# Performance work log

Hardware: AMD Instinct MI355X
Metric: run time of the kernel (lower is better)

Reference implementation:

```python
import jax, jax.numpy as jnp
import numpy as np

N_IN = 512
SCALE = 0  # s / n_in**scale == s when scale=0

def setup_inputs() -> dict:
    key = jax.random.key(0)
    k1, k2, k3, k4 = jax.random.split(key, 4)
    B, S, D = 4, 128, N_IN
    x = jax.random.normal(k1, (B, S, D), dtype=jnp.float32)
    y = jax.random.normal(k2, (B, S, D), dtype=jnp.float32)
    z = jax.random.normal(k3, (B, S, D), dtype=jnp.float32)
    # weight: (n_out, n_in + bias_x, n_in, n_in + bias_y)
    weight = jax.random.normal(k4, (1, D + 1, D, D + 1), dtype=jnp.float32) * 0.02
    return {"x": x, "y": y, "z": z, "weight": weight}

def reference(x, y, z, weight):
    # append bias-1 column to x and y (bias_x=bias_y=True)
    ones = jnp.ones_like(x[..., :1])
    xb = jnp.concatenate([x, ones], axis=-1)           # [b, s, n_in+1]
    yb = jnp.concatenate([y, jnp.ones_like(y[..., :1])], axis=-1)
    # w = z^T W : [b, o, z, i, j]
    w = jnp.einsum('bzk,oikj->bozij', z, weight)
    # s(x,y,z) = x^T (z^T W) y : [b, o, z, x, y]
    s = jnp.einsum('bxi,bozij,byj->bozxy', xb, w, yb)
    # n_out == 1 -> squeeze channel dim; scale == 0 -> divide by n_in**0 == 1
    return jnp.squeeze(s, axis=1) / (N_IN ** SCALE)
```

## Files before the change

### kernel.cpp

```cpp
#include <hip/hip_runtime.h>
#include <stdint.h>


typedef __attribute__((ext_vector_type(8))) short bf16x8;
typedef __attribute__((ext_vector_type(4))) float f32x4;

__device__ __forceinline__ unsigned short f2bf(float f) {
    unsigned int u = __float_as_uint(f);
    u += 0x7fffu + ((u >> 16) & 1u);
    return (unsigned short)(u >> 16);
}

__device__ __forceinline__ void gload_lds16(const void* g, void* l) {
    __builtin_amdgcn_global_load_lds((const __attribute__((address_space(1))) void*)g,
                                     (__attribute__((address_space(3))) void*)l, 16, 0, 0);
}

__global__ __launch_bounds__(256) void k_cast(const float* __restrict__ x,
    const float* __restrict__ y, const float* __restrict__ z,
    unsigned short* __restrict__ xbf, unsigned short* __restrict__ ybf,
    unsigned short* __restrict__ zbf)
{
    int t = blockIdx.x * 256 + threadIdx.x;
    int arr = t >> 15;
    int off = (t & 32767) * 8;
    const float* src = (arr == 0) ? x : (arr == 1) ? y : z;
    unsigned short* dst = (arr == 0) ? xbf : (arr == 1) ? ybf : zbf;
    float4 a = *(const float4*)(src + off);
    float4 b = *(const float4*)(src + off + 4);
    uint4 o;
    o.x = f2bf(a.x) | ((unsigned)f2bf(a.y) << 16);
    o.y = f2bf(a.z) | ((unsigned)f2bf(a.w) << 16);
    o.z = f2bf(b.x) | ((unsigned)f2bf(b.y) << 16);
    o.w = f2bf(b.z) | ((unsigned)f2bf(b.w) << 16);
    *(uint4*)(dst + off) = o;
}

__global__ __launch_bounds__(256) void k_edge(const float* __restrict__ z,
    const float* __restrict__ w, float* __restrict__ a_arr,
    float* __restrict__ c_arr, float* __restrict__ d_arr)
{
    __shared__ float Zs[64][33];
    __shared__ float Bs[32][65];
    int t = threadIdx.x;
    int mb = blockIdx.x % 17, bzb = blockIdx.x / 17;
    int tr = t >> 4, tc = t & 15;
    float acc[4][4] = {};
    for (int k0 = 0; k0 < 512; k0 += 32) {
        __syncthreads();
        {   int row = t >> 2, ko = (t & 3) * 8;
            const float* p = z + (bzb * 64 + row) * 512 + k0 + ko;
            float4 v0 = ((const float4*)p)[0], v1 = ((const float4*)p)[1];
            Zs[row][ko + 0] = v0.x; Zs[row][ko + 1] = v0.y; Zs[row][ko + 2] = v0.z; Zs[row][ko + 3] = v0.w;
            Zs[row][ko + 4] = v1.x; Zs[row][ko + 5] = v1.y; Zs[row][ko + 6] = v1.z; Zs[row][ko + 7] = v1.w;
        }
        {   int kr = t >> 3, mo = (t & 7) * 8;
            for (int e = 0; e < 8; ++e) {
                int m = mb * 64 + mo + e;
                float v = 0.f;
                int krow = k0 + kr;
                if (m < 512)        v = w[(m * 512 + krow) * 513 + 512];
                else if (m < 1024)  v = w[(262144 + krow) * 513 + (m - 512)];
                else if (m == 1024) v = w[(262144 + krow) * 513 + 512];
                Bs[kr][mo + e] = v;
            }
        }
        __syncthreads();
        for (int kk = 0; kk < 32; ++kk) {
            float zr[4], br[4];
            for (int r = 0; r < 4; ++r) zr[r] = Zs[tr * 4 + r][kk];
            for (int c = 0; c < 4; ++c) br[c] = Bs[kk][tc * 4 + c];
            for (int r = 0; r < 4; ++r)
                for (int c = 0; c < 4; ++c) acc[r][c] += zr[r] * br[c];
        }
    }
    for (int r = 0; r < 4; ++r)
        for (int c = 0; c < 4; ++c) {
            int bz = bzb * 64 + tr * 4 + r;
            int m = mb * 64 + tc * 4 + c;
            if (m < 512)        a_arr[bz * 512 + m] = acc[r][c];
            else if (m < 1024)  c_arr[bz * 512 + (m - 512)] = acc[r][c];
            else if (m == 1024) d_arr[bz] = acc[r][c];
        }
}

__global__ __launch_bounds__(512, 2) void k_gemm1(const unsigned short* __restrict__ zbf,
    const float* __restrict__ w, unsigned short* __restrict__ Mws,
    int i0, int chi)
{
    extern __shared__ unsigned char smem[];
    unsigned char* Zb0 = smem;
    unsigned char* Zb1 = smem + 32768;
    unsigned char* Bb0 = smem + 65536;
    unsigned char* Bb1 = smem + 73728;

    int nwg = gridDim.x;
    int cpx = nwg >> 3;
    int bid = blockIdx.x;
    int swz = (bid & 7) * cpx + (bid >> 3);
    int iloc = swz >> 2, jb = swz & 3;
    int j0 = jb * 128;
    int t = threadIdx.x, wid = t >> 6, lane = t & 63;
    int bzg = wid >> 1, jg = wid & 1;
    int l15 = lane & 15, l4 = lane >> 4;

    int arow = lane >> 2;
    int akc  = (lane & 3) ^ ((lane >> 3) & 3);
    const unsigned short* zbase = zbf + (size_t)(wid * 64 + arow) * 512 + akc * 8;

    int jB = t & 127, kq8 = t >> 7;
    const float* wb = w + (size_t)(i0 + iloc) * 262656 + (size_t)(kq8 * 8) * 513 + j0 + jB;
    int bwoff = jB * 64 + (((kq8 >> 1) ^ ((jB >> 1) & 3)) * 16) + 0;
    bwoff = jB * 64 + ((kq8 ^ ((jB >> 1) & 3)) * 16);

    int aoff = (bzg * 128 + l15) * 64 + ((l4 ^ ((l15 >> 1) & 3)) * 16);
    int boff = (jg * 64 + l15) * 64 + ((l4 ^ ((l15 >> 1) & 3)) * 16);

    f32x4 acc[8][4];
    #pragma unroll
    for (int mt = 0; mt < 8; ++mt)
        #pragma unroll
        for (int nt = 0; nt < 4; ++nt) acc[mt][nt] = (f32x4){0.f, 0.f, 0.f, 0.f};

    float wr[2][8];

    #pragma unroll
    for (int q = 0; q < 4; ++q)
        gload_lds16(zbase + q * 8192, Zb0 + wid * 4096 + q * 1024);
    {
        #pragma unroll
        for (int e = 0; e < 8; ++e) wr[0][e] = wb[(size_t)e * 513];
        const float* wp = wb + (size_t)32 * 513;
        #pragma unroll
        for (int e = 0; e < 8; ++e) wr[1][e] = wp[(size_t)e * 513];
        uint4 pk;
        pk.x = f2bf(wr[0][0]) | ((unsigned)f2bf(wr[0][1]) << 16);
        pk.y = f2bf(wr[0][2]) | ((unsigned)f2bf(wr[0][3]) << 16);
        pk.z = f2bf(wr[0][4]) | ((unsigned)f2bf(wr[0][5]) << 16);
        pk.w = f2bf(wr[0][6]) | ((unsigned)f2bf(wr[0][7]) << 16);
        *(uint4*)(Bb0 + bwoff) = pk;
    }
    asm volatile("s_waitcnt lgkmcnt(0)" ::: "memory");
    __builtin_amdgcn_s_barrier();
    __builtin_amdgcn_sched_barrier(0);

    #pragma unroll
    for (int ks = 0; ks < 16; ++ks) {
        const int cur = ks & 1;
        unsigned char* Zcur  = cur ? Zb1 : Zb0;
        unsigned char* Znext = cur ? Zb0 : Zb1;
        unsigned char* Bcur  = cur ? Bb1 : Bb0;
        unsigned char* Bnext = cur ? Bb0 : Bb1;

        if (ks < 15) {
            #pragma unroll
            for (int q = 0; q < 4; ++q)
                gload_lds16(zbase + (ks + 1) * 32 + q * 8192, Znext + wid * 4096 + q * 1024);
        }
        if (ks < 14) {
            const float* wp = wb + (size_t)(ks + 2) * 32 * 513;
            #pragma unroll
            for (int e = 0; e < 8; ++e) wr[cur][e] = wp[(size_t)e * 513];
        }
        bf16x8 bfr[4];
        #pragma unroll
        for (int nt = 0; nt < 4; ++nt)
            bfr[nt] = *(const bf16x8*)(Bcur + boff + nt * 1024);
        #pragma unroll
        for (int mt = 0; mt < 8; ++mt) {
            bf16x8 afr = *(const bf16x8*)(Zcur + aoff + mt * 1024);
            #pragma unroll
            for (int nt = 0; nt < 4; ++nt)
                acc[mt][nt] = __builtin_amdgcn_mfma_f32_16x16x32_bf16(afr, bfr[nt], acc[mt][nt], 0, 0, 0);
        }
        if (ks < 15) {
            uint4 pk;
            pk.x = f2bf(wr[cur ^ 1][0]) | ((unsigned)f2bf(wr[cur ^ 1][1]) << 16);
            pk.y = f2bf(wr[cur ^ 1][2]) | ((unsigned)f2bf(wr[cur ^ 1][3]) << 16);
            pk.z = f2bf(wr[cur ^ 1][4]) | ((unsigned)f2bf(wr[cur ^ 1][5]) << 16);
            pk.w = f2bf(wr[cur ^ 1][6]) | ((unsigned)f2bf(wr[cur ^ 1][7]) << 16);
            *(uint4*)(Bnext + bwoff) = pk;
        }
        if (ks < 14) {
            asm volatile("s_waitcnt vmcnt(8) lgkmcnt(0)" ::: "memory");
        } else if (ks == 14) {
            asm volatile("s_waitcnt vmcnt(0) lgkmcnt(0)" ::: "memory");
        }
        if (ks < 15) {
            __builtin_amdgcn_s_barrier();
            __builtin_amdgcn_sched_barrier(0);
        }
    }

    size_t mrow = (size_t)chi * 512;
    #pragma unroll
    for (int mt = 0; mt < 8; ++mt)
        #pragma unroll
        for (int nt = 0; nt < 4; ++nt)
            #pragma unroll
            for (int r = 0; r < 4; ++r) {
                int bz = bzg * 128 + mt * 16 + l4 * 4 + r;
                int j  = j0 + jg * 64 + nt * 16 + l15;
                Mws[(size_t)bz * mrow + (size_t)iloc * 512 + j] = f2bf(acc[mt][nt][r]);
            }
}

__global__ __launch_bounds__(512) void k_fuse(const unsigned short* __restrict__ xbf,
    const unsigned short* __restrict__ ybf, const unsigned short* __restrict__ Mws,
    const float* __restrict__ xf, const float* __restrict__ yf,
    const float* __restrict__ a_arr, const float* __restrict__ c_arr,
    const float* __restrict__ d_arr, float* __restrict__ out,
    int i0, int nib, int chi, int first)
{
    __shared__ unsigned short Xlds[128 * 72];
    __shared__ unsigned short Ylds[128 * 72];
    __shared__ unsigned short Mlds[64 * 72];
    __shared__ unsigned short Rlds[128 * 72];
    int bid = blockIdx.x;
    int bz = (bid & 7) * 64 + (bid >> 3);
    int b = bz >> 7;
    int t = threadIdx.x;
    int wid = t >> 6, lane = t & 63;
    int l15 = lane & 15, l4 = lane >> 4;
    int xg = wid >> 2, yg = wid & 3;

    f32x4 acc[4][2];
    if (first) {
        float* part = (float*)Xlds;
        float* uv = (float*)Ylds;
        int xr = t & 127, q = t >> 7;
        {   const float* xp = xf + (size_t)(b * 128 + xr) * 512 + q * 128;
            const float* ap = a_arr + bz * 512 + q * 128;
            float s = 0.f;
            for (int ii = 0; ii < 128; ++ii) s += xp[ii] * ap[ii];
            part[q * 128 + xr] = s;
        }
        __syncthreads();
        if (t < 128) uv[t] = part[t] + part[128 + t] + part[256 + t] + part[384 + t];
        __syncthreads();
        {   const float* yp = yf + (size_t)(b * 128 + xr) * 512 + q * 128;
            const float* cp = c_arr + bz * 512 + q * 128;
            float s = 0.f;
            for (int ii = 0; ii < 128; ++ii) s += yp[ii] * cp[ii];
            part[q * 128 + xr] = s;
        }
        __syncthreads();
        if (t < 128) uv[128 + t] = part[t] + part[128 + t] + part[256 + t] + part[384 + t];
        __syncthreads();
        float dv = d_arr[bz];
        for (int mt = 0; mt < 4; ++mt)
            for (int nt = 0; nt < 2; ++nt) {
                int y = yg * 32 + nt * 16 + l15;
                for (int r = 0; r < 4; ++r) {
                    int x = xg * 64 + mt * 16 + l4 * 4 + r;
                    acc[mt][nt][r] = uv[x] + uv[128 + y] + dv;
                }
            }
    } else {
        for (int mt = 0; mt < 4; ++mt) for (int nt = 0; nt < 2; ++nt) acc[mt][nt] = (f32x4){0.f,0.f,0.f,0.f};
    }

    for (int ibl = 0; ibl < nib; ++ibl) {
        __syncthreads();
        {   int xr = t >> 2, io = (t & 3) * 16;
            const uint4* src = (const uint4*)(xbf + (size_t)(b * 128 + xr) * 512 + i0 + ibl * 64 + io);
            uint4 v0 = src[0], v1 = src[1];
            uint4* dst = (uint4*)(Xlds + xr * 72 + io);
            dst[0] = v0; dst[1] = v1;
        }
        f32x4 accR[2][2];
        for (int mt = 0; mt < 2; ++mt) for (int nt = 0; nt < 2; ++nt) accR[mt][nt] = (f32x4){0.f,0.f,0.f,0.f};

        for (int jbk = 0; jbk < 8; ++jbk) {
            __syncthreads();
            {   int yr = t >> 2, jo = (t & 3) * 16;
                const uint4* src = (const uint4*)(ybf + (size_t)(b * 128 + yr) * 512 + jbk * 64 + jo);
                uint4 v0 = src[0], v1 = src[1];
                uint4* dst = (uint4*)(Ylds + yr * 72 + jo);
                dst[0] = v0; dst[1] = v1;
            }
            {   int ir = t >> 3, jo = (t & 7) * 8;
                uint4 v = *(const uint4*)(Mws + (size_t)bz * ((size_t)chi * 512)
                                              + (size_t)(ibl * 64 + ir) * 512 + jbk * 64 + jo);
                *(uint4*)(Mlds + ir * 72 + jo) = v;
            }
            __syncthreads();
            for (int kf = 0; kf < 2; ++kf) {
                bf16x8 bfr[2];
                for (int nt = 0; nt < 2; ++nt) {
                    int y = yg * 32 + nt * 16 + l15;
                    bfr[nt] = *(const bf16x8*)(Ylds + y * 72 + kf * 32 + l4 * 8);
                }
                for (int mt = 0; mt < 2; ++mt) {
                    int ir = xg * 32 + mt * 16 + l15;
                    bf16x8 afr = *(const bf16x8*)(Mlds + ir * 72 + kf * 32 + l4 * 8);
                    accR[mt][0] = __builtin_amdgcn_mfma_f32_16x16x32_bf16(afr, bfr[0], accR[mt][0], 0, 0, 0);
                    accR[mt][1] = __builtin_amdgcn_mfma_f32_16x16x32_bf16(afr, bfr[1], accR[mt][1], 0, 0, 0);
                }
            }
        }
        for (int mt = 0; mt < 2; ++mt)
            for (int nt = 0; nt < 2; ++nt) {
                int y = yg * 32 + nt * 16 + l15;
                int ir = xg * 32 + mt * 16 + l4 * 4;
                unsigned p0 = f2bf(accR[mt][nt][0]) | ((unsigned)f2bf(accR[mt][nt][1]) << 16);
                unsigned p1 = f2bf(accR[mt][nt][2]) | ((unsigned)f2bf(accR[mt][nt][3]) << 16);
                *(uint2*)(Rlds + y * 72 + ir) = make_uint2(p0, p1);
            }
        __syncthreads();
        for (int kf = 0; kf < 2; ++kf) {
            bf16x8 bfr[2];
            for (int nt = 0; nt < 2; ++nt) {
                int y = yg * 32 + nt * 16 + l15;
                bfr[nt] = *(const bf16x8*)(Rlds + y * 72 + kf * 32 + l4 * 8);
            }
            for (int mt = 0; mt < 4; ++mt) {
                int x = xg * 64 + mt * 16 + l15;
                bf16x8 afr = *(const bf16x8*)(Xlds + x * 72 + kf * 32 + l4 * 8);
                acc[mt][0] = __builtin_amdgcn_mfma_f32_16x16x32_bf16(afr, bfr[0], acc[mt][0], 0, 0, 0);
                acc[mt][1] = __builtin_amdgcn_mfma_f32_16x16x32_bf16(afr, bfr[1], acc[mt][1], 0, 0, 0);
            }
        }
    }
    float* op = out + (size_t)bz * 16384;
    for (int mt = 0; mt < 4; ++mt)
        for (int nt = 0; nt < 2; ++nt)
            for (int r = 0; r < 4; ++r) {
                int x = xg * 64 + mt * 16 + l4 * 4 + r;
                int y = yg * 32 + nt * 16 + l15;
                if (first) op[x * 128 + y] = acc[mt][nt][r];
                else       op[x * 128 + y] += acc[mt][nt][r];
            }
}

extern "C" void kernel_launch(void* const* d_in, const int* in_sizes, int n_in,
                              void* d_out, int out_size, void* d_ws, size_t ws_size,
                              hipStream_t stream)
{
    const float* x = (const float*)d_in[0];
    const float* y = (const float*)d_in[1];
    const float* z = (const float*)d_in[2];
    const float* w = (const float*)d_in[3];
    float* out = (float*)d_out;
    char* ws = (char*)d_ws;

    unsigned short* xbf = (unsigned short*)(ws + 0);
    unsigned short* ybf = (unsigned short*)(ws + 524288);
    unsigned short* zbf = (unsigned short*)(ws + 1048576);
    float* a_arr = (float*)(ws + 1572864);
    float* c_arr = (float*)(ws + 2621440);
    float* d_arr = (float*)(ws + 3670016);
    unsigned short* Mws = (unsigned short*)(ws + 3674112);

    size_t avail = (ws_size > 3674112) ? ws_size - 3674112 : 0;
    int chi = 512;
    while (chi > 64 && (size_t)chi * 524288 > avail) chi >>= 1;

    hipLaunchKernelGGL(k_cast, dim3(384), dim3(256), 0, stream, x, y, z, xbf, ybf, zbf);
    hipLaunchKernelGGL(k_edge, dim3(136), dim3(256), 0, stream, z, w, a_arr, c_arr, d_arr);

    int nch = 512 / chi;
    for (int c = 0; c < nch; ++c) {
        int i0 = c * chi;
        hipLaunchKernelGGL(k_gemm1, dim3(chi * 4), dim3(512), 81920, stream, zbf, w, Mws, i0, chi);
        hipLaunchKernelGGL(k_fuse, dim3(512), dim3(512), 0, stream, xbf, ybf, Mws,
                           x, y, a_arr, c_arr, d_arr, out, i0, chi / 64, chi, (c == 0) ? 1 : 0);
    }
}
```

Before: 543.1 us.

## Restructure k_fuse with double-buffered async LDS loads and larger i-blocks

Rewrites the fused second stage so Y and M tiles are fetched with direct global-to-LDS loads into double buffers, overlapping the next tile's fetch with the current MFMA work. The i-block grows from 64 to 128, the warp tiling changes to 2x4 fragments per wave, and the padded LDS layouts are replaced by XOR-swizzled ones to avoid bank conflicts. It uses 128 KB of dynamic shared memory and a launch bound of two blocks, which may limit occupancy. The minimum chunk size rises to 128 so that chi/128 stays integral.

```diff
diff --git a/kernel.cpp b/kernel.cpp
--- a/kernel.cpp
+++ b/kernel.cpp
@@ -110,8 +110,7 @@
 
     int jB = t & 127, kq8 = t >> 7;
     const float* wb = w + (size_t)(i0 + iloc) * 262656 + (size_t)(kq8 * 8) * 513 + j0 + jB;
-    int bwoff = jB * 64 + (((kq8 >> 1) ^ ((jB >> 1) & 3)) * 16) + 0;
-    bwoff = jB * 64 + ((kq8 ^ ((jB >> 1) & 3)) * 16);
+    int bwoff = jB * 64 + ((kq8 ^ ((jB >> 1) & 3)) * 16);
 
     int aoff = (bzg * 128 + l15) * 64 + ((l4 ^ ((l15 >> 1) & 3)) * 16);
     int boff = (jg * 64 + l15) * 64 + ((l4 ^ ((l15 >> 1) & 3)) * 16);
@@ -205,29 +204,44 @@
             }
 }
 
-__global__ __launch_bounds__(512) void k_fuse(const unsigned short* __restrict__ xbf,
+__global__ __launch_bounds__(512, 2) void k_fuse(const unsigned short* __restrict__ xbf,
     const unsigned short* __restrict__ ybf, const unsigned short* __restrict__ Mws,
     const float* __restrict__ xf, const float* __restrict__ yf,
     const float* __restrict__ a_arr, const float* __restrict__ c_arr,
     const float* __restrict__ d_arr, float* __restrict__ out,
     int i0, int nib, int chi, int first)
 {
-    __shared__ unsigned short Xlds[128 * 72];
-    __shared__ unsigned short Ylds[128 * 72];
-    __shared__ unsigned short Mlds[64 * 72];
-    __shared__ unsigned short Rlds[128 * 72];
+    extern __shared__ unsigned char smem[];
+    unsigned char* Yb = smem;
+    unsigned char* Mb = smem + 32768;
+    unsigned char* Xl = smem + 65536;
+    unsigned char* Rl = smem + 98304;
+
     int bid = blockIdx.x;
     int bz = (bid & 7) * 64 + (bid >> 3);
     int b = bz >> 7;
     int t = threadIdx.x;
     int wid = t >> 6, lane = t & 63;
     int l15 = lane & 15, l4 = lane >> 4;
-    int xg = wid >> 2, yg = wid & 3;
-
-    f32x4 acc[4][2];
+    int g4 = wid >> 1, g2 = wid & 1;
+
+    int srow = t >> 3;
+    int sj16 = (t & 7) ^ ((t >> 3) & 7);
+    int xrow = t >> 4;
+    int xi16 = (t & 15) ^ ((t >> 4) & 15);
+    size_t bzoff = (size_t)bz * ((size_t)chi * 512);
+    const unsigned short* ybase = ybf + (size_t)(b * 128) * 512;
+    const unsigned short* xbase = xbf + (size_t)(b * 128) * 512;
+
+    f32x4 acc[2][4];
+    gload_lds16(ybase + (size_t)srow * 512 + sj16 * 8, Yb + t * 16);
+    gload_lds16(ybase + (size_t)(64 + srow) * 512 + sj16 * 8, Yb + 8192 + t * 16);
+    gload_lds16(Mws + bzoff + (size_t)srow * 512 + sj16 * 8, Mb + t * 16);
+    gload_lds16(Mws + bzoff + (size_t)(64 + srow) * 512 + sj16 * 8, Mb + 8192 + t * 16);
+
     if (first) {
-        float* part = (float*)Xlds;
-        float* uv = (float*)Ylds;
+        float* part = (float*)Rl;
+        float* uv = (float*)(Rl + 4096);
         int xr = t & 127, q = t >> 7;
         {   const float* xp = xf + (size_t)(b * 128 + xr) * 512 + q * 128;
             const float* ap = a_arr + bz * 512 + q * 128;
@@ -248,86 +262,132 @@
         if (t < 128) uv[128 + t] = part[t] + part[128 + t] + part[256 + t] + part[384 + t];
         __syncthreads();
         float dv = d_arr[bz];
-        for (int mt = 0; mt < 4; ++mt)
-            for (int nt = 0; nt < 2; ++nt) {
-                int y = yg * 32 + nt * 16 + l15;
+        #pragma unroll
+        for (int mt = 0; mt < 2; ++mt)
+            #pragma unroll
+            for (int nt = 0; nt < 4; ++nt) {
+                int y = g2 * 64 + nt * 16 + l15;
+                #pragma unroll
                 for (int r = 0; r < 4; ++r) {
-                    int x = xg * 64 + mt * 16 + l4 * 4 + r;
+                    int x = g4 * 32 + mt * 16 + l4 * 4 + r;
                     acc[mt][nt][r] = uv[x] + uv[128 + y] + dv;
                 }
             }
     } else {
-        for (int mt = 0; mt < 4; ++mt) for (int nt = 0; nt < 2; ++nt) acc[mt][nt] = (f32x4){0.f,0.f,0.f,0.f};
-    }
-
+        #pragma unroll
+        for (int mt = 0; mt < 2; ++mt)
+            #pragma unroll
+            for (int nt = 0; nt < 4; ++nt) acc[mt][nt] = (f32x4){0.f,0.f,0.f,0.f};
+    }
+    asm volatile("s_waitcnt vmcnt(0) lgkmcnt(0)" ::: "memory");
+    __builtin_amdgcn_s_barrier();
+    __builtin_amdgcn_sched_barrier(0);
+
+    int NF = nib * 8;
     for (int ibl = 0; ibl < nib; ++ibl) {
-        __syncthreads();
-        {   int xr = t >> 2, io = (t & 3) * 16;
-            const uint4* src = (const uint4*)(xbf + (size_t)(b * 128 + xr) * 512 + i0 + ibl * 64 + io);
-            uint4 v0 = src[0], v1 = src[1];
-            uint4* dst = (uint4*)(Xlds + xr * 72 + io);
-            dst[0] = v0; dst[1] = v1;
-        }
-        f32x4 accR[2][2];
-        for (int mt = 0; mt < 2; ++mt) for (int nt = 0; nt < 2; ++nt) accR[mt][nt] = (f32x4){0.f,0.f,0.f,0.f};
-
-        for (int jbk = 0; jbk < 8; ++jbk) {
-            __syncthreads();
-            {   int yr = t >> 2, jo = (t & 3) * 16;
-                const uint4* src = (const uint4*)(ybf + (size_t)(b * 128 + yr) * 512 + jbk * 64 + jo);
-                uint4 v0 = src[0], v1 = src[1];
-                uint4* dst = (uint4*)(Ylds + yr * 72 + jo);
-                dst[0] = v0; dst[1] = v1;
-            }
-            {   int ir = t >> 3, jo = (t & 7) * 8;
-                uint4 v = *(const uint4*)(Mws + (size_t)bz * ((size_t)chi * 512)
-                                              + (size_t)(ibl * 64 + ir) * 512 + jbk * 64 + jo);
-                *(uint4*)(Mlds + ir * 72 + jo) = v;
-            }
-            __syncthreads();
+        f32x4 accR[2][4];
+        #pragma unroll
+        for (int mt = 0; mt < 2; ++mt)
+            #pragma unroll
+            for (int nt = 0; nt < 4; ++nt) accR[mt][nt] = (f32x4){0.f,0.f,0.f,0.f};
+
+        #pragma unroll
+        for (int s = 0; s < 8; ++s) {
+            int f = ibl * 8 + s;
+            const int cur = s & 1;
+            unsigned char* Ycur = Yb + cur * 16384;
+            unsigned char* Mcur = Mb + cur * 16384;
+            unsigned char* Ynxt = Yb + (cur ^ 1) * 16384;
+            unsigned char* Mnxt = Mb + (cur ^ 1) * 16384;
+
+            if (f + 1 < NF) {
+                int jn = ((f + 1) & 7) * 64;
+                int rn = ((f + 1) >> 3) * 128;
+                gload_lds16(ybase + (size_t)srow * 512 + jn + sj16 * 8, Ynxt + t * 16);
+                gload_lds16(ybase + (size_t)(64 + srow) * 512 + jn + sj16 * 8, Ynxt + 8192 + t * 16);
+                gload_lds16(Mws + bzoff + (size_t)(rn + srow) * 512 + jn + sj16 * 8, Mnxt + t * 16);
+                gload_lds16(Mws + bzoff + (size_t)(rn + 64 + srow) * 512 + jn + sj16 * 8, Mnxt + 8192 + t * 16);
+            }
+            if (s == 0) {
+                #pragma unroll
+                for (int q = 0; q < 4; ++q)
+                    gload_lds16(xbase + (size_t)(q * 32 + xrow) * 512 + i0 + ibl * 128 + xi16 * 8,
+                                Xl + q * 8192 + t * 16);
+            }
+            #pragma unroll
             for (int kf = 0; kf < 2; ++kf) {
-                bf16x8 bfr[2];
-                for (int nt = 0; nt < 2; ++nt) {
-                    int y = yg * 32 + nt * 16 + l15;
-                    bfr[nt] = *(const bf16x8*)(Ylds + y * 72 + kf * 32 + l4 * 8);
+                bf16x8 bfr[4], afr[2];
+                #pragma unroll
+                for (int nt = 0; nt < 4; ++nt) {
+                    int y = g2 * 64 + nt * 16 + l15;
+                    bfr[nt] = *(const bf16x8*)(Ycur + y * 128 + (((kf * 4 + l4) ^ (y & 7)) * 16));
                 }
+                #pragma unroll
                 for (int mt = 0; mt < 2; ++mt) {
-                    int ir = xg * 32 + mt * 16 + l15;
-                    bf16x8 afr = *(const bf16x8*)(Mlds + ir * 72 + kf * 32 + l4 * 8);
-                    accR[mt][0] = __builtin_amdgcn_mfma_f32_16x16x32_bf16(afr, bfr[0], accR[mt][0], 0, 0, 0);
-                    accR[mt][1] = __builtin_amdgcn_mfma_f32_16x16x32_bf16(afr, bfr[1], accR[mt][1], 0, 0, 0);
+                    int ir = g4 * 32 + mt * 16 + l15;
+                    afr[mt] = *(const bf16x8*)(Mcur + ir * 128 + (((kf * 4 + l4) ^ (ir & 7)) * 16));
                 }
-            }
-        }
+                #pragma unroll
+                for (int mt = 0; mt < 2; ++mt)
+                    #pragma unroll
+                    for (int nt = 0; nt < 4; ++nt)
+                        accR[mt][nt] = __builtin_amdgcn_mfma_f32_16x16x32_bf16(afr[mt], bfr[nt], accR[mt][nt], 0, 0, 0);
+            }
+            asm volatile("s_waitcnt vmcnt(0) lgkmcnt(0)" ::: "memory");
+            __builtin_amdgcn_s_barrier();
+            __builtin_amdgcn_sched_barrier(0);
+        }
+
+        #pragma unroll
         for (int mt = 0; mt < 2; ++mt)
-            for (int nt = 0; nt < 2; ++nt) {
-                int y = yg * 32 + nt * 16 + l15;
-                int ir = xg * 32 + mt * 16 + l4 * 4;
+            #pragma unroll
+            for (int nt = 0; nt < 4; ++nt) {
+                int y = g2 * 64 + nt * 16 + l15;
+                int ib = g4 * 32 + mt * 16 + l4 * 4;
                 unsigned p0 = f2bf(accR[mt][nt][0]) | ((unsigned)f2bf(accR[mt][nt][1]) << 16);
                 unsigned p1 = f2bf(accR[mt][nt][2]) | ((unsigned)f2bf(accR[mt][nt][3]) << 16);
-                *(uint2*)(Rlds + y * 72 + ir) = make_uint2(p0, p1);
-            }
-        __syncthreads();
-        for (int kf = 0; kf < 2; ++kf) {
-            bf16x8 bfr[2];
-            for (int nt = 0; nt < 2; ++nt) {
-                int y = yg * 32 + nt * 16 + l15;
-                bfr[nt] = *(const bf16x8*)(Rlds + y * 72 + kf * 32 + l4 * 8);
-            }
-            for (int mt = 0; mt < 4; ++mt) {
-                int x = xg * 64 + mt * 16 + l15;
-                bf16x8 afr = *(const bf16x8*)(Xlds + x * 72 + kf * 32 + l4 * 8);
-                acc[mt][0] = __builtin_amdgcn_mfma_f32_16x16x32_bf16(afr, bfr[0], acc[mt][0], 0, 0, 0);
-                acc[mt][1] = __builtin_amdgcn_mfma_f32_16x16x32_bf16(afr, bfr[1], acc[mt][1], 0, 0, 0);
-            }
-        }
-    }
+                int byte = y * 256 + (((ib >> 3) ^ (y & 15)) * 16) + ((ib & 4) << 1);
+                *(uint2*)(Rl + byte) = make_uint2(p0, p1);
+            }
+        asm volatile("s_waitcnt lgkmcnt(0)" ::: "memory");
+        __builtin_amdgcn_s_barrier();
+        __builtin_amdgcn_sched_barrier(0);
+
+        #pragma unroll
+        for (int kf = 0; kf < 4; ++kf) {
+            bf16x8 bfr[4], afr[2];
+            #pragma unroll
+            for (int nt = 0; nt < 4; ++nt) {
+                int y = g2 * 64 + nt * 16 + l15;
+                bfr[nt] = *(const bf16x8*)(Rl + y * 256 + (((kf * 4 + l4) ^ (y & 15)) * 16));
+            }
+            #pragma unroll
+            for (int mt = 0; mt < 2; ++mt) {
+                int xr = g4 * 32 + mt * 16 + l15;
+                afr[mt] = *(const bf16x8*)(Xl + xr * 256 + (((kf * 4 + l4) ^ (xr & 15)) * 16));
+            }
+            #pragma unroll
+            for (int mt = 0; mt < 2; ++mt)
+                #pragma unroll
+                for (int nt = 0; nt < 4; ++nt)
+                    acc[mt][nt] = __builtin_amdgcn_mfma_f32_16x16x32_bf16(afr[mt], bfr[nt], acc[mt][nt], 0, 0, 0);
+        }
+        if (ibl + 1 < nib) {
+            asm volatile("s_waitcnt lgkmcnt(0)" ::: "memory");
+            __builtin_amdgcn_s_barrier();
+            __builtin_amdgcn_sched_barrier(0);
+        }
+    }
+
     float* op = out + (size_t)bz * 16384;
-    for (int mt = 0; mt < 4; ++mt)
-        for (int nt = 0; nt < 2; ++nt)
+    #pragma unroll
+    for (int mt = 0; mt < 2; ++mt)
+        #pragma unroll
+        for (int nt = 0; nt < 4; ++nt)
+            #pragma unroll
             for (int r = 0; r < 4; ++r) {
-                int x = xg * 64 + mt * 16 + l4 * 4 + r;
-                int y = yg * 32 + nt * 16 + l15;
+                int x = g4 * 32 + mt * 16 + l4 * 4 + r;
+                int y = g2 * 64 + nt * 16 + l15;
                 if (first) op[x * 128 + y] = acc[mt][nt][r];
                 else       op[x * 128 + y] += acc[mt][nt][r];
             }
@@ -354,7 +414,7 @@
 
     size_t avail = (ws_size > 3674112) ? ws_size - 3674112 : 0;
     int chi = 512;
-    while (chi > 64 && (size_t)chi * 524288 > avail) chi >>= 1;
+    while (chi > 128 && (size_t)chi * 524288 > avail) chi >>= 1;
 
     hipLaunchKernelGGL(k_cast, dim3(384), dim3(256), 0, stream, x, y, z, xbf, ybf, zbf);
     hipLaunchKernelGGL(k_edge, dim3(136), dim3(256), 0, stream, z, w, a_arr, c_arr, d_arr);
@@ -363,7 +423,7 @@
     for (int c = 0; c < nch; ++c) {
         int i0 = c * chi;
         hipLaunchKernelGGL(k_gemm1, dim3(chi * 4), dim3(512), 81920, stream, zbf, w, Mws, i0, chi);
-        hipLaunchKernelGGL(k_fuse, dim3(512), dim3(512), 0, stream, xbf, ybf, Mws,
-                           x, y, a_arr, c_arr, d_arr, out, i0, chi / 64, chi, (c == 0) ? 1 : 0);
-    }
-}
+        hipLaunchKernelGGL(k_fuse, dim3(512), dim3(512), 131072, stream, xbf, ybf, Mws,
+                           x, y, a_arr, c_arr, d_arr, out, i0, chi / 128, chi, (c == 0) ? 1 : 0);
+    }
+}
```

Measured after the change: 484.7 us. 10.8% less time.

## Drop chunking; load A fragments directly to registers; restructure fuse kernel per bz

Applied to the files above, without the earlier changes.

The gemm1 kernel now reads z fragments straight from global memory into registers instead of staging them in LDS, which shrinks its LDS use to the B double buffer. Chunking over i is removed, so gemm1 always launches 2048 blocks and the fuse kernel runs once. The fuse kernel is restructured: each block loads all of y into a swizzled 128KB LDS buffer, computes the full M·y product with register-prefetched M fragments, writes R back into the same LDS, then multiplies by x fragments taken from global memory. The aim is fewer barriers and launches and less LDS staging. The cost is higher register pressure, and the code now assumes the workspace can hold the full 256MB M buffer with no fallback.

```diff
diff --git a/kernel.cpp b/kernel.cpp
--- a/kernel.cpp
+++ b/kernel.cpp
@@ -85,17 +85,13 @@
 }
 
 __global__ __launch_bounds__(512, 2) void k_gemm1(const unsigned short* __restrict__ zbf,
-    const float* __restrict__ w, unsigned short* __restrict__ Mws,
-    int i0, int chi)
+    const float* __restrict__ w, unsigned short* __restrict__ Mws)
 {
     extern __shared__ unsigned char smem[];
-    unsigned char* Zb0 = smem;
-    unsigned char* Zb1 = smem + 32768;
-    unsigned char* Bb0 = smem + 65536;
-    unsigned char* Bb1 = smem + 73728;
-
-    int nwg = gridDim.x;
-    int cpx = nwg >> 3;
+    unsigned char* Bb0 = smem;
+    unsigned char* Bb1 = smem + 8192;
+
+    int nwg = gridDim.x, cpx = nwg >> 3;
     int bid = blockIdx.x;
     int swz = (bid & 7) * cpx + (bid >> 3);
     int iloc = swz >> 2, jb = swz & 3;
@@ -104,16 +100,11 @@
     int bzg = wid >> 1, jg = wid & 1;
     int l15 = lane & 15, l4 = lane >> 4;
 
-    int arow = lane >> 2;
-    int akc  = (lane & 3) ^ ((lane >> 3) & 3);
-    const unsigned short* zbase = zbf + (size_t)(wid * 64 + arow) * 512 + akc * 8;
+    const unsigned short* abase = zbf + (size_t)(bzg * 128 + l15) * 512 + l4 * 8;
 
     int jB = t & 127, kq8 = t >> 7;
-    const float* wb = w + (size_t)(i0 + iloc) * 262656 + (size_t)(kq8 * 8) * 513 + j0 + jB;
-    int bwoff = jB * 64 + (((kq8 >> 1) ^ ((jB >> 1) & 3)) * 16) + 0;
-    bwoff = jB * 64 + ((kq8 ^ ((jB >> 1) & 3)) * 16);
-
-    int aoff = (bzg * 128 + l15) * 64 + ((l4 ^ ((l15 >> 1) & 3)) * 16);
+    const float* wb = w + (size_t)iloc * 262656 + (size_t)(kq8 * 8) * 513 + j0 + jB;
+    int bwoff = jB * 64 + ((kq8 ^ ((jB >> 1) & 3)) * 16);
     int boff = (jg * 64 + l15) * 64 + ((l4 ^ ((l15 >> 1) & 3)) * 16);
 
     f32x4 acc[8][4];
@@ -122,11 +113,12 @@
         #pragma unroll
         for (int nt = 0; nt < 4; ++nt) acc[mt][nt] = (f32x4){0.f, 0.f, 0.f, 0.f};
 
+    bf16x8 ar[2][8];
     float wr[2][8];
 
     #pragma unroll
-    for (int q = 0; q < 4; ++q)
-        gload_lds16(zbase + q * 8192, Zb0 + wid * 4096 + q * 1024);
+    for (int mt = 0; mt < 8; ++mt)
+        ar[0][mt] = *(const bf16x8*)(abase + (size_t)mt * 8192);
     {
         #pragma unroll
         for (int e = 0; e < 8; ++e) wr[0][e] = wb[(size_t)e * 513];
@@ -147,15 +139,13 @@
     #pragma unroll
     for (int ks = 0; ks < 16; ++ks) {
         const int cur = ks & 1;
-        unsigned char* Zcur  = cur ? Zb1 : Zb0;
-        unsigned char* Znext = cur ? Zb0 : Zb1;
         unsigned char* Bcur  = cur ? Bb1 : Bb0;
         unsigned char* Bnext = cur ? Bb0 : Bb1;
 
         if (ks < 15) {
             #pragma unroll
-            for (int q = 0; q < 4; ++q)
-                gload_lds16(zbase + (ks + 1) * 32 + q * 8192, Znext + wid * 4096 + q * 1024);
+            for (int mt = 0; mt < 8; ++mt)
+                ar[cur ^ 1][mt] = *(const bf16x8*)(abase + (size_t)mt * 8192 + (ks + 1) * 32);
         }
         if (ks < 14) {
             const float* wp = wb + (size_t)(ks + 2) * 32 * 513;
@@ -168,10 +158,9 @@
             bfr[nt] = *(const bf16x8*)(Bcur + boff + nt * 1024);
         #pragma unroll
         for (int mt = 0; mt < 8; ++mt) {
-            bf16x8 afr = *(const bf16x8*)(Zcur + aoff + mt * 1024);
             #pragma unroll
             for (int nt = 0; nt < 4; ++nt)
-                acc[mt][nt] = __builtin_amdgcn_mfma_f32_16x16x32_bf16(afr, bfr[nt], acc[mt][nt], 0, 0, 0);
+                acc[mt][nt] = __builtin_amdgcn_mfma_f32_16x16x32_bf16(ar[cur][mt], bfr[nt], acc[mt][nt], 0, 0, 0);
         }
         if (ks < 15) {
             uint4 pk;
@@ -181,18 +170,13 @@
             pk.w = f2bf(wr[cur ^ 1][6]) | ((unsigned)f2bf(wr[cur ^ 1][7]) << 16);
             *(uint4*)(Bnext + bwoff) = pk;
         }
-        if (ks < 14) {
-            asm volatile("s_waitcnt vmcnt(8) lgkmcnt(0)" ::: "memory");
-        } else if (ks == 14) {
-            asm volatile("s_waitcnt vmcnt(0) lgkmcnt(0)" ::: "memory");
-        }
         if (ks < 15) {
+            asm volatile("s_waitcnt lgkmcnt(0)" ::: "memory");
             __builtin_amdgcn_s_barrier();
             __builtin_amdgcn_sched_barrier(0);
         }
     }
 
-    size_t mrow = (size_t)chi * 512;
     #pragma unroll
     for (int mt = 0; mt < 8; ++mt)
         #pragma unroll
@@ -201,33 +185,37 @@
             for (int r = 0; r < 4; ++r) {
                 int bz = bzg * 128 + mt * 16 + l4 * 4 + r;
                 int j  = j0 + jg * 64 + nt * 16 + l15;
-                Mws[(size_t)bz * mrow + (size_t)iloc * 512 + j] = f2bf(acc[mt][nt][r]);
-            }
-}
-
-__global__ __launch_bounds__(512) void k_fuse(const unsigned short* __restrict__ xbf,
+                Mws[(size_t)bz * 262144 + (size_t)iloc * 512 + j] = f2bf(acc[mt][nt][r]);
+            }
+}
+
+__global__ __launch_bounds__(512, 2) void k_fuse(const unsigned short* __restrict__ xbf,
     const unsigned short* __restrict__ ybf, const unsigned short* __restrict__ Mws,
     const float* __restrict__ xf, const float* __restrict__ yf,
     const float* __restrict__ a_arr, const float* __restrict__ c_arr,
-    const float* __restrict__ d_arr, float* __restrict__ out,
-    int i0, int nib, int chi, int first)
-{
-    __shared__ unsigned short Xlds[128 * 72];
-    __shared__ unsigned short Ylds[128 * 72];
-    __shared__ unsigned short Mlds[64 * 72];
-    __shared__ unsigned short Rlds[128 * 72];
+    const float* __restrict__ d_arr, float* __restrict__ out)
+{
+    extern __shared__ unsigned char smem[];
+    __shared__ float part[512];
+    __shared__ float uv[256];
+
     int bid = blockIdx.x;
     int bz = (bid & 7) * 64 + (bid >> 3);
     int b = bz >> 7;
-    int t = threadIdx.x;
-    int wid = t >> 6, lane = t & 63;
+    int t = threadIdx.x, wid = t >> 6, lane = t & 63;
     int l15 = lane & 15, l4 = lane >> 4;
     int xg = wid >> 2, yg = wid & 3;
-
-    f32x4 acc[4][2];
-    if (first) {
-        float* part = (float*)Xlds;
-        float* uv = (float*)Ylds;
+    int g8 = wid;
+
+    const unsigned short* ybase = ybf + (size_t)(b * 128) * 512;
+    #pragma unroll
+    for (int it = 0; it < 16; ++it) {
+        int row = it * 8 + wid;
+        gload_lds16(ybase + (size_t)row * 512 + ((lane ^ (row & 63)) * 8),
+                    smem + it * 8192 + t * 16);
+    }
+
+    {
         int xr = t & 127, q = t >> 7;
         {   const float* xp = xf + (size_t)(b * 128 + xr) * 512 + q * 128;
             const float* ap = a_arr + bz * 512 + q * 128;
@@ -247,89 +235,115 @@
         __syncthreads();
         if (t < 128) uv[128 + t] = part[t] + part[128 + t] + part[256 + t] + part[384 + t];
         __syncthreads();
-        float dv = d_arr[bz];
+    }
+    float dv = d_arr[bz];
+    f32x4 acc[4][2];
+    #pragma unroll
+    for (int mt = 0; mt < 4; ++mt)
+        #pragma unroll
+        for (int nt = 0; nt < 2; ++nt) {
+            int y = yg * 32 + nt * 16 + l15;
+            #pragma unroll
+            for (int r = 0; r < 4; ++r) {
+                int x = xg * 64 + mt * 16 + l4 * 4 + r;
+                acc[mt][nt][r] = uv[x] + uv[128 + y] + dv;
+            }
+        }
+
+    const unsigned short* mbase = Mws + (size_t)bz * 262144
+                                + (size_t)(g8 * 64 + l15) * 512 + l4 * 8;
+    f32x4 accR[4][8];
+    #pragma unroll
+    for (int mt = 0; mt < 4; ++mt)
+        #pragma unroll
+        for (int nt = 0; nt < 8; ++nt) accR[mt][nt] = (f32x4){0.f, 0.f, 0.f, 0.f};
+
+    bf16x8 mfr[2][4];
+    #pragma unroll
+    for (int mt = 0; mt < 4; ++mt) {
+        mfr[0][mt] = *(const bf16x8*)(mbase + (size_t)mt * 8192);
+        mfr[1][mt] = *(const bf16x8*)(mbase + (size_t)mt * 8192 + 32);
+    }
+    #pragma unroll
+    for (int kf = 0; kf < 16; ++kf) {
+        #pragma unroll
+        for (int nh = 0; nh < 2; ++nh) {
+            bf16x8 yfr[4];
+            #pragma unroll
+            for (int n4 = 0; n4 < 4; ++n4) {
+                int y = (nh * 4 + n4) * 16 + l15;
+                yfr[n4] = *(const bf16x8*)(smem + y * 1024 + (((kf * 4 + l4) ^ (y & 63)) * 16));
+            }
+            #pragma unroll
+            for (int mt = 0; mt < 4; ++mt)
+                #pragma unroll
+                for (int n4 = 0; n4 < 4; ++n4)
+                    accR[mt][nh * 4 + n4] = __builtin_amdgcn_mfma_f32_16x16x32_bf16(
+                        mfr[kf & 1][mt], yfr[n4], accR[mt][nh * 4 + n4], 0, 0, 0);
+        }
+        if (kf < 14) {
+            #pragma unroll
+            for (int mt = 0; mt < 4; ++mt)
+                mfr[kf & 1][mt] = *(const bf16x8*)(mbase + (size_t)mt * 8192 + (kf + 2) * 32);
+        }
+    }
+    asm volatile("s_waitcnt lgkmcnt(0)" ::: "memory");
+    __builtin_amdgcn_s_barrier();
+    __builtin_amdgcn_sched_barrier(0);
+
+    #pragma unroll
+    for (int mt = 0; mt < 4; ++mt)
+        #pragma unroll
+        for (int nt = 0; nt < 8; ++nt) {
+            int y = nt * 16 + l15;
+            int chunk = g8 * 8 + mt * 2 + (l4 >> 1);
+            int byte = y * 1024 + ((chunk ^ (y & 63)) * 16) + (l4 & 1) * 8;
+            unsigned p0 = f2bf(accR[mt][nt][0]) | ((unsigned)f2bf(accR[mt][nt][1]) << 16);
+            unsigned p1 = f2bf(accR[mt][nt][2]) | ((unsigned)f2bf(accR[mt][nt][3]) << 16);
+            *(uint2*)(smem + byte) = make_uint2(p0, p1);
+        }
+    asm volatile("s_waitcnt lgkmcnt(0)" ::: "memory");
+    __builtin_amdgcn_s_barrier();
+    __builtin_amdgcn_sched_barrier(0);
+
+    const unsigned short* xbase = xbf + (size_t)(b * 128 + xg * 64 + l15) * 512 + l4 * 8;
+    bf16x8 xfr[2][4];
+    #pragma unroll
+    for (int mt = 0; mt < 4; ++mt) {
+        xfr[0][mt] = *(const bf16x8*)(xbase + (size_t)mt * 8192);
+        xfr[1][mt] = *(const bf16x8*)(xbase + (size_t)mt * 8192 + 32);
+    }
+    #pragma unroll
+    for (int kf = 0; kf < 16; ++kf) {
+        bf16x8 rfr[2];
+        #pragma unroll
+        for (int nt = 0; nt < 2; ++nt) {
+            int y = yg * 32 + nt * 16 + l15;
+            rfr[nt] = *(const bf16x8*)(smem + y * 1024 + (((kf * 4 + l4) ^ (y & 63)) * 16));
+        }
+        #pragma unroll
         for (int mt = 0; mt < 4; ++mt)
-            for (int nt = 0; nt < 2; ++nt) {
-                int y = yg * 32 + nt * 16 + l15;
-                for (int r = 0; r < 4; ++r) {
-                    int x = xg * 64 + mt * 16 + l4 * 4 + r;
-                    acc[mt][nt][r] = uv[x] + uv[128 + y] + dv;
-                }
-            }
-    } else {
-        for (int mt = 0; mt < 4; ++mt) for (int nt = 0; nt < 2; ++nt) acc[mt][nt] = (f32x4){0.f,0.f,0.f,0.f};
-    }
-
-    for (int ibl = 0; ibl < nib; ++ibl) {
-        __syncthreads();
-        {   int xr = t >> 2, io = (t & 3) * 16;
-            const uint4* src = (const uint4*)(xbf + (size_t)(b * 128 + xr) * 512 + i0 + ibl * 64 + io);
-            uint4 v0 = src[0], v1 = src[1];
-            uint4* dst = (uint4*)(Xlds + xr * 72 + io);
-            dst[0] = v0; dst[1] = v1;
-        }
-        f32x4 accR[2][2];
-        for (int mt = 0; mt < 2; ++mt) for (int nt = 0; nt < 2; ++nt) accR[mt][nt] = (f32x4){0.f,0.f,0.f,0.f};
-
-        for (int jbk = 0; jbk < 8; ++jbk) {
-            __syncthreads();
-            {   int yr = t >> 2, jo = (t & 3) * 16;
-                const uint4* src = (const uint4*)(ybf + (size_t)(b * 128 + yr) * 512 + jbk * 64 + jo);
-                uint4 v0 = src[0], v1 = src[1];
-                uint4* dst = (uint4*)(Ylds + yr * 72 + jo);
-                dst[0] = v0; dst[1] = v1;
-            }
-            {   int ir = t >> 3, jo = (t & 7) * 8;
-                uint4 v = *(const uint4*)(Mws + (size_t)bz * ((size_t)chi * 512)
-                                              + (size_t)(ibl * 64 + ir) * 512 + jbk * 64 + jo);
-                *(uint4*)(Mlds + ir * 72 + jo) = v;
-            }
-            __syncthreads();
-            for (int kf = 0; kf < 2; ++kf) {
-                bf16x8 bfr[2];
-                for (int nt = 0; nt < 2; ++nt) {
-                    int y = yg * 32 + nt * 16 + l15;
-                    bfr[nt] = *(const bf16x8*)(Ylds + y * 72 + kf * 32 + l4 * 8);
-                }
-                for (int mt = 0; mt < 2; ++mt) {
-                    int ir = xg * 32 + mt * 16 + l15;
-                    bf16x8 afr = *(const bf16x8*)(Mlds + ir * 72 + kf * 32 + l4 * 8);
-                    accR[mt][0] = __builtin_amdgcn_mfma_f32_16x16x32_bf16(afr, bfr[0], accR[mt][0], 0, 0, 0);
-                    accR[mt][1] = __builtin_amdgcn_mfma_f32_16x16x32_bf16(afr, bfr[1], accR[mt][1], 0, 0, 0);
-                }
-            }
-        }
-        for (int mt = 0; mt < 2; ++mt)
-            for (int nt = 0; nt < 2; ++nt) {
-                int y = yg * 32 + nt * 16 + l15;
-                int ir = xg * 32 + mt * 16 + l4 * 4;
-                unsigned p0 = f2bf(accR[mt][nt][0]) | ((unsigned)f2bf(accR[mt][nt][1]) << 16);
-                unsigned p1 = f2bf(accR[mt][nt][2]) | ((unsigned)f2bf(accR[mt][nt][3]) << 16);
-                *(uint2*)(Rlds + y * 72 + ir) = make_uint2(p0, p1);
-            }
-        __syncthreads();
-        for (int kf = 0; kf < 2; ++kf) {
-            bf16x8 bfr[2];
-            for (int nt = 0; nt < 2; ++nt) {
-                int y = yg * 32 + nt * 16 + l15;
-                bfr[nt] = *(const bf16x8*)(Rlds + y * 72 + kf * 32 + l4 * 8);
-            }
-            for (int mt = 0; mt < 4; ++mt) {
-                int x = xg * 64 + mt * 16 + l15;
-                bf16x8 afr = *(const bf16x8*)(Xlds + x * 72 + kf * 32 + l4 * 8);
-                acc[mt][0] = __builtin_amdgcn_mfma_f32_16x16x32_bf16(afr, bfr[0], acc[mt][0], 0, 0, 0);
-                acc[mt][1] = __builtin_amdgcn_mfma_f32_16x16x32_bf16(afr, bfr[1], acc[mt][1], 0, 0, 0);
-            }
-        }
-    }
+            #pragma unroll
+            for (int nt = 0; nt < 2; ++nt)
+                acc[mt][nt] = __builtin_amdgcn_mfma_f32_16x16x32_bf16(
+                    xfr[kf & 1][mt], rfr[nt], acc[mt][nt], 0, 0, 0);
+        if (kf < 14) {
+            #pragma unroll
+            for (int mt = 0; mt < 4; ++mt)
+                xfr[kf & 1][mt] = *(const bf16x8*)(xbase + (size_t)mt * 8192 + (kf + 2) * 32);
+        }
+    }
+
     float* op = out + (size_t)bz * 16384;
+    #pragma unroll
     for (int mt = 0; mt < 4; ++mt)
+        #pragma unroll
         for (int nt = 0; nt < 2; ++nt)
+            #pragma unroll
             for (int r = 0; r < 4; ++r) {
                 int x = xg * 64 + mt * 16 + l4 * 4 + r;
                 int y = yg * 32 + nt * 16 + l15;
-                if (first) op[x * 128 + y] = acc[mt][nt][r];
-                else       op[x * 128 + y] += acc[mt][nt][r];
+                op[x * 128 + y] = acc[mt][nt][r];
             }
 }
 
@@ -352,18 +366,9 @@
     float* d_arr = (float*)(ws + 3670016);
     unsigned short* Mws = (unsigned short*)(ws + 3674112);
 
-    size_t avail = (ws_size > 3674112) ? ws_size - 3674112 : 0;
-    int chi = 512;
-    while (chi > 64 && (size_t)chi * 524288 > avail) chi >>= 1;
-
     hipLaunchKernelGGL(k_cast, dim3(384), dim3(256), 0, stream, x, y, z, xbf, ybf, zbf);
     hipLaunchKernelGGL(k_edge, dim3(136), dim3(256), 0, stream, z, w, a_arr, c_arr, d_arr);
-
-    int nch = 512 / chi;
-    for (int c = 0; c < nch; ++c) {
-        int i0 = c * chi;
-        hipLaunchKernelGGL(k_gemm1, dim3(chi * 4), dim3(512), 81920, stream, zbf, w, Mws, i0, chi);
-        hipLaunchKernelGGL(k_fuse, dim3(512), dim3(512), 0, stream, xbf, ybf, Mws,
-                           x, y, a_arr, c_arr, d_arr, out, i0, chi / 64, chi, (c == 0) ? 1 : 0);
-    }
-}
+    hipLaunchKernelGGL(k_gemm1, dim3(2048), dim3(512), 16384, stream, zbf, w, Mws);
+    hipLaunchKernelGGL(k_fuse, dim3(512), dim3(512), 131072, stream, xbf, ybf, Mws,
+                       x, y, a_arr, c_arr, d_arr, out);
+}
```

Result: slower. 606.5 us (+11.7%).
